# Optimization experiments

Measured on AMD Instinct MI355X. Metric: run time of the kernel, lower is better.

Reference implementation:

```python
import jax, jax.numpy as jnp
import numpy as np

VOCAB = 50001; W2V = 300; S2V = 256; HID = 256; COUT = 256; NTAG = 4; NHEADS = 5
N_POSTS = 2048; SEQ = 64


def mha(x, wqkv, bqkv, wo, bo, h):
    # torch nn.MultiheadAttention (batch_first, eval mode, no mask)
    n, s, d = x.shape
    hd = d // h
    qkv = x @ wqkv.T + bqkv                      # [n, s, 3d]
    q, k, v = jnp.split(qkv, 3, axis=-1)
    rs = lambda t: t.reshape(n, s, h, hd).transpose(0, 2, 1, 3)  # [n, h, s, hd]
    q, k, v = rs(q), rs(k), rs(v)
    att = jax.nn.softmax(jnp.einsum('nhqd,nhkd->nhqk', q, k) * (hd ** -0.5), axis=-1)
    o = jnp.einsum('nhqk,nhkd->nhqd', att, v).transpose(0, 2, 1, 3).reshape(n, s, d)
    return o @ wo.T + bo


def gcn_conv(x, ei, w, b):
    n = x.shape[0]
    loops = jnp.arange(n)
    src = jnp.concatenate([ei[0], loops])
    dst = jnp.concatenate([ei[1], loops])
    deg = jax.ops.segment_sum(jnp.ones(dst.shape[0], dtype=x.dtype), dst, num_segments=n)
    dinv = jnp.where(deg > 0, jax.lax.rsqrt(deg), 0.0)
    norm = dinv[src] * dinv[dst]                 # [E+n]
    h = x @ w.T                                  # [n, out]
    return jax.ops.segment_sum(norm[:, None] * h[src], dst, num_segments=n) + b


def gcn_branch(x, ei, root, w1, b1, w2, b2):
    # GCN.forward: conv1 -> cat root feat -> relu -> conv2 -> relu -> cat conv1 root -> mean
    n = x.shape[0]
    c1 = gcn_conv(x, ei, w1, b1)                 # [n, HID]
    post_root = jnp.broadcast_to(x[root], (n, x.shape[1]))
    c2_in = jax.nn.relu(jnp.concatenate([c1, post_root], axis=1))
    c2 = jax.nn.relu(gcn_conv(c2_in, ei, w2, b2))
    c1_root = jnp.broadcast_to(c1[root], (n, c1.shape[1]))
    feat = jnp.concatenate([c1_root, c2], axis=1)  # [n, HID+COUT]
    return jnp.mean(feat, axis=0).reshape(1, -1)


def setup_inputs() -> dict:
    key = jax.random.key(0)
    ks = jax.random.split(key, 16)
    p = lambda i, shp, sc=0.02: jax.random.normal(ks[i], shp, dtype=jnp.float32) * sc
    return {
        'nodeText': jax.random.randint(ks[0], (N_POSTS, SEQ), 0, VOCAB),
        'edgeIndexTD': jax.random.randint(ks[1], (2, N_POSTS - 1), 0, N_POSTS),
        'edgeIndexBU': jax.random.randint(ks[2], (2, N_POSTS - 1), 0, N_POSTS),
        'threadIndex': 0,
        'mission': 1,
        'embed_w': p(3, (VOCAB, W2V), 1.0),
        'in_proj_w': p(4, (3 * W2V, W2V)),
        'in_proj_b': jnp.zeros((3 * W2V,), jnp.float32),
        'out_proj_w': p(5, (W2V, W2V)),
        'out_proj_b': jnp.zeros((W2V,), jnp.float32),
        's2v_w': p(6, (S2V, W2V)),
        's2v_b': jnp.zeros((S2V,), jnp.float32),
        'td_w1': p(7, (HID, S2V)), 'td_b1': jnp.zeros((HID,), jnp.float32),
        'td_w2': p(8, (COUT, HID + S2V)), 'td_b2': jnp.zeros((COUT,), jnp.float32),
        'bu_w1': p(9, (HID, S2V)), 'bu_b1': jnp.zeros((HID,), jnp.float32),
        'bu_w2': p(10, (COUT, HID + S2V)), 'bu_b2': jnp.zeros((COUT,), jnp.float32),
        'fc_w': p(11, (NTAG, (COUT + HID) * 2)),
        'fc_b': jnp.zeros((NTAG,), jnp.float32),
    }


def reference(nodeText, edgeIndexTD, edgeIndexBU, threadIndex, mission,
              embed_w, in_proj_w, in_proj_b, out_proj_w, out_proj_b,
              s2v_w, s2v_b, td_w1, td_b1, td_w2, td_b2,
              bu_w1, bu_b1, bu_w2, bu_b2, fc_w, fc_b):
    # ABGCN.forward, mission == 1 (rumor/BiGCN path), eval mode (dropout off)
    nf = embed_w[nodeText]                                  # [N, S, W2V]
    nf = mha(nf, in_proj_w, in_proj_b, out_proj_w, out_proj_b, NHEADS)
    nf = jnp.tanh(nf @ s2v_w.T + s2v_b)                     # [N, S, S2V]
    s2v = nf[:, 0, :]                                       # first token per post
    td = gcn_branch(s2v, edgeIndexTD, threadIndex, td_w1, td_b1, td_w2, td_b2)
    bu = gcn_branch(s2v, edgeIndexBU, threadIndex, bu_w1, bu_b1, bu_w2, bu_b2)
    return jnp.concatenate([td, bu], axis=1) @ fc_w.T + fc_b  # [1, NTAG]
```

## Files before the change

kernel.cpp:

```cpp
#include <hip/hip_runtime.h>

#define NPOSTS 2048
#define SEQ 64
#define W2V 300
#define NH 5
#define HD 60
#define S2VD 256
#define HIDD 256
#define NEDGE 2047
#define UDIM 1500

#define GLOAD_LDS(g, l) \
    __builtin_amdgcn_global_load_lds((const __attribute__((address_space(1))) void*)(g), \
                                     (__attribute__((address_space(3))) void*)(l), 16, 0, 0)

__global__ __launch_bounds__(320) void k_wfoldA(
    const float* __restrict__ Ws, const float* __restrict__ Wo,
    const float* __restrict__ bo, const float* __restrict__ bs,
    float* __restrict__ WsWo, float* __restrict__ bias3A)
{
    const int r0 = blockIdx.x * 16;
    const int tid = threadIdx.x;
    __shared__ float sT[W2V][16];
    for (int i = tid; i < 16 * W2V; i += 320) {
        int r = i / W2V, k = i % W2V;
        sT[k][r] = Ws[(size_t)(r0 + r) * W2V + k];
    }
    __syncthreads();
    if (tid <= W2V) {
        float a[16];
        #pragma unroll
        for (int r = 0; r < 16; ++r) a[r] = 0.f;
        for (int k = 0; k < W2V; ++k) {
            float wv = (tid < W2V) ? Wo[(size_t)k * W2V + tid] : bo[k];
            const float4* s4 = reinterpret_cast<const float4*>(&sT[k][0]);
            float4 q0 = s4[0], q1 = s4[1], q2 = s4[2], q3 = s4[3];
            float qq[16] = {q0.x,q0.y,q0.z,q0.w, q1.x,q1.y,q1.z,q1.w,
                            q2.x,q2.y,q2.z,q2.w, q3.x,q3.y,q3.z,q3.w};
            #pragma unroll
            for (int r = 0; r < 16; ++r) a[r] = fmaf(wv, qq[r], a[r]);
        }
        if (tid < W2V) {
            #pragma unroll
            for (int r = 0; r < 16; ++r) WsWo[(size_t)(r0 + r) * W2V + tid] = a[r];
        } else {
            #pragma unroll
            for (int r = 0; r < 16; ++r) bias3A[r0 + r] = bs[r0 + r] + a[r];
        }
    }
}

__global__ __launch_bounds__(320) void k_wfold2(
    const float* __restrict__ WsWo, const float* __restrict__ Wqkv, const float* __restrict__ bqkv,
    float* __restrict__ Wfold, float* __restrict__ bpart)
{
    const int r0 = blockIdx.x * 16;
    const int h = blockIdx.y;
    const int tid = threadIdx.x;
    __shared__ float sT[HD][16];
    for (int i = tid; i < 16 * HD; i += 320) {
        int r = i / HD, d = i % HD;
        sT[d][r] = WsWo[(size_t)(r0 + r) * W2V + h * HD + d];
    }
    __syncthreads();
    if (tid <= W2V) {
        float a[16];
        #pragma unroll
        for (int r = 0; r < 16; ++r) a[r] = 0.f;
        for (int d = 0; d < HD; ++d) {
            float wv = (tid < W2V) ? Wqkv[(size_t)(2 * W2V + h * HD + d) * W2V + tid]
                                   : bqkv[2 * W2V + h * HD + d];
            const float4* s4 = reinterpret_cast<const float4*>(&sT[d][0]);
            float4 q0 = s4[0], q1 = s4[1], q2 = s4[2], q3 = s4[3];
            float qq[16] = {q0.x,q0.y,q0.z,q0.w, q1.x,q1.y,q1.z,q1.w,
                            q2.x,q2.y,q2.z,q2.w, q3.x,q3.y,q3.z,q3.w};
            #pragma unroll
            for (int r = 0; r < 16; ++r) a[r] = fmaf(wv, qq[r], a[r]);
        }
        if (tid < W2V) {
            #pragma unroll
            for (int r = 0; r < 16; ++r)
                Wfold[(size_t)(r0 + r) * UDIM + h * W2V + tid] = a[r];
        } else {
            #pragma unroll
            for (int r = 0; r < 16; ++r) bpart[h * S2VD + r0 + r] = a[r];
        }
    }
}

__global__ __launch_bounds__(320) void k_q(
    const int* __restrict__ nodeText, const float* __restrict__ embed_w,
    const float* __restrict__ Wqkv, const float* __restrict__ bqkv,
    float* __restrict__ Qout)
{
    const int r0 = blockIdx.x * 8;
    const int tid = threadIdx.x;
    __shared__ int stok[8];
    __shared__ float sE[8][W2V];
    if (tid < 8) stok[tid] = nodeText[(size_t)(r0 + tid) * SEQ];
    __syncthreads();
    for (int i = tid; i < 8 * 75; i += 320) {
        int r = i / 75, c4 = i % 75;
        *reinterpret_cast<float4*>(&sE[r][c4 * 4]) =
            *reinterpret_cast<const float4*>(embed_w + (size_t)stok[r] * W2V + c4 * 4);
    }
    __syncthreads();
    if (tid < W2V) {
        const float4* w4p = reinterpret_cast<const float4*>(Wqkv + (size_t)tid * W2V);
        float b = bqkv[tid];
        float a[8];
        #pragma unroll
        for (int r = 0; r < 8; ++r) a[r] = b;
        for (int c4 = 0; c4 < 75; ++c4) {
            float4 w4 = w4p[c4];
            #pragma unroll
            for (int r = 0; r < 8; ++r) {
                float4 v = *reinterpret_cast<const float4*>(&sE[r][c4 * 4]);
                a[r] = fmaf(w4.x, v.x, a[r]);
                a[r] = fmaf(w4.y, v.y, a[r]);
                a[r] = fmaf(w4.z, v.z, a[r]);
                a[r] = fmaf(w4.w, v.w, a[r]);
            }
        }
        #pragma unroll
        for (int r = 0; r < 8; ++r) Qout[(size_t)(r0 + r) * W2V + tid] = a[r];
    }
}

__global__ __launch_bounds__(320) void k_u(
    const float* __restrict__ Q, const float* __restrict__ Wqkv, float* __restrict__ uout)
{
    const int r0 = blockIdx.x * 16;
    const int h = blockIdx.y;
    const int tid = threadIdx.x;
    __shared__ float sT[HD][16];
    for (int i = tid; i < 16 * HD; i += 320) {
        int r = i / HD, d = i % HD;
        sT[d][r] = Q[(size_t)(r0 + r) * W2V + h * HD + d];
    }
    __syncthreads();
    if (tid < W2V) {
        float a[16];
        #pragma unroll
        for (int r = 0; r < 16; ++r) a[r] = 0.f;
        for (int d = 0; d < HD; ++d) {
            float wv = Wqkv[(size_t)(W2V + h * HD + d) * W2V + tid];
            const float4* s4 = reinterpret_cast<const float4*>(&sT[d][0]);
            float4 q0 = s4[0], q1 = s4[1], q2 = s4[2], q3 = s4[3];
            float qq[16] = {q0.x,q0.y,q0.z,q0.w, q1.x,q1.y,q1.z,q1.w,
                            q2.x,q2.y,q2.z,q2.w, q3.x,q3.y,q3.z,q3.w};
            #pragma unroll
            for (int r = 0; r < 16; ++r) a[r] = fmaf(wv, qq[r], a[r]);
        }
        #pragma unroll
        for (int r = 0; r < 16; ++r)
            uout[(size_t)(r0 + r) * UDIM + h * W2V + tid] = a[r];
    }
}

__global__ __launch_bounds__(512) void k_att(
    const int* __restrict__ nodeText, const float* __restrict__ embed_w,
    float* __restrict__ ue)
{
    __shared__ float sE[2 * SEQ * W2V];
    __shared__ float satt[2][NH][SEQ];
    __shared__ int   stoks[2][SEQ];

    const int p0 = blockIdx.x * 2;
    const int tid = threadIdx.x;
    const int wave = tid >> 6, lane = tid & 63;

    if (tid < 2 * SEQ) stoks[tid >> 6][tid & 63] = nodeText[(size_t)p0 * SEQ + tid];
    __syncthreads();

    #pragma unroll 3
    for (int it = 0; it < 18; ++it) {
        int i = it * 512 + tid;
        int pp = i / 4800, idx = i % 4800;
        int row = idx / 75, c4 = idx - row * 75;
        const float* src = embed_w + (size_t)stoks[pp][row] * W2V + c4 * 4;
        GLOAD_LDS(src, &sE[i * 4]);
    }
    if (wave < 6) {
        int i = 18 * 512 + tid;
        int pp = i / 4800, idx = i % 4800;
        int row = idx / 75, c4 = idx - row * 75;
        const float* src = embed_w + (size_t)stoks[pp][row] * W2V + c4 * 4;
        GLOAD_LDS(src, &sE[i * 4]);
    }
    asm volatile("s_waitcnt vmcnt(0)" ::: "memory");
    __syncthreads();

    const float SC = 0.12909944487358056f;
    for (int task = wave; task < 2 * NH; task += 8) {
        int pp = task / NH, h = task - pp * NH;
        const float4* u4 = reinterpret_cast<const float4*>(ue + (size_t)(p0 + pp) * UDIM + h * W2V);
        const float* er = &sE[(pp * SEQ + lane) * W2V];
        float acc = 0.f;
        #pragma unroll 5
        for (int c4 = 0; c4 < 75; ++c4) {
            float4 uv = u4[c4];
            float4 ev = *reinterpret_cast<const float4*>(er + c4 * 4);
            acc = fmaf(uv.x, ev.x, acc);
            acc = fmaf(uv.y, ev.y, acc);
            acc = fmaf(uv.z, ev.z, acc);
            acc = fmaf(uv.w, ev.w, acc);
        }
        float ex = expf(acc * SC);
        float l = ex;
        #pragma unroll
        for (int off = 32; off > 0; off >>= 1) l += __shfl_xor(l, off);
        satt[pp][h][lane] = ex / l;
    }
    __syncthreads();

    for (int t = tid; t < 2 * NH * 75; t += 512) {
        int pp = t / 375, r = t - pp * 375;
        int h = r / 75, c4 = r - h * 75;
        const float* att = &satt[pp][h][0];
        const float* eb = &sE[pp * SEQ * W2V + c4 * 4];
        float4 a = make_float4(0.f, 0.f, 0.f, 0.f);
        #pragma unroll 4
        for (int j = 0; j < SEQ; ++j) {
            float av = att[j];
            float4 ev = *reinterpret_cast<const float4*>(eb + j * W2V);
            a.x = fmaf(av, ev.x, a.x);
            a.y = fmaf(av, ev.y, a.y);
            a.z = fmaf(av, ev.z, a.z);
            a.w = fmaf(av, ev.w, a.w);
        }
        *reinterpret_cast<float4*>(ue + (size_t)(p0 + pp) * UDIM + h * W2V + c4 * 4) = a;
    }
}

__global__ __launch_bounds__(256) void k_s2v(
    const float* __restrict__ e, const float* __restrict__ Wfold,
    const float* __restrict__ bias3A, const float* __restrict__ bpart,
    float* __restrict__ s2v_out)
{
    const int r0 = blockIdx.x * 8;
    const int t = threadIdx.x;
    __shared__ float se[8][W2V];
    float a[8];
    #pragma unroll
    for (int r = 0; r < 8; ++r) a[r] = 0.f;
    const float bias = bias3A[t] + bpart[t] + bpart[256 + t] + bpart[512 + t]
                     + bpart[768 + t] + bpart[1024 + t];
    const float4* w4p = reinterpret_cast<const float4*>(Wfold + (size_t)t * UDIM);
    for (int ch = 0; ch < 5; ++ch) {
        __syncthreads();
        for (int i = t; i < 8 * 75; i += 256) {
            int r = i / 75, c4 = i % 75;
            *reinterpret_cast<float4*>(&se[r][c4 * 4]) =
                *reinterpret_cast<const float4*>(e + (size_t)(r0 + r) * UDIM + ch * W2V + c4 * 4);
        }
        __syncthreads();
        for (int c4 = 0; c4 < 75; ++c4) {
            float4 w4 = w4p[ch * 75 + c4];
            #pragma unroll
            for (int r = 0; r < 8; ++r) {
                float4 v = *reinterpret_cast<const float4*>(&se[r][c4 * 4]);
                a[r] = fmaf(w4.x, v.x, a[r]);
                a[r] = fmaf(w4.y, v.y, a[r]);
                a[r] = fmaf(w4.z, v.z, a[r]);
                a[r] = fmaf(w4.w, v.w, a[r]);
            }
        }
    }
    #pragma unroll
    for (int r = 0; r < 8; ++r)
        s2v_out[(size_t)(r0 + r) * S2VD + t] = tanhf(a[r] + bias);
}


__global__ __launch_bounds__(256) void k_deg(
    const int* __restrict__ eiTD, const int* __restrict__ eiBU, int* __restrict__ deg)
{
    const int b = blockIdx.y;
    const int* ei = b ? eiBU : eiTD;
    int e = blockIdx.x * 256 + threadIdx.x;
    if (e < NEDGE) atomicAdd(&deg[b * NPOSTS + ei[NEDGE + e]], 1);
}

__global__ __launch_bounds__(256) void k_gemm1(
    const float* __restrict__ x, const float* __restrict__ wtd, const float* __restrict__ wbu,
    const float* __restrict__ btd, const float* __restrict__ bbu, const int* __restrict__ deg,
    float* __restrict__ hout, float* __restrict__ cout_)
{
    const int b = blockIdx.y;
    const float* w = b ? wbu : wtd;
    const float* bias = b ? bbu : btd;
    float* hb = hout + (size_t)b * NPOSTS * HIDD;
    float* cb = cout_ + (size_t)b * NPOSTS * HIDD;
    const int* dg = deg + b * NPOSTS;
    const int r0 = blockIdx.x * 16;
    const int tid = threadIdx.x;
    __shared__ float sx[16][S2VD];
    for (int i = tid; i < 16 * S2VD; i += 256)
        sx[i / S2VD][i % S2VD] = x[(size_t)(r0 + i / S2VD) * S2VD + (i % S2VD)];
    __syncthreads();
    float acc[16];
    #pragma unroll
    for (int r = 0; r < 16; ++r) acc[r] = 0.f;
    const float4* wr4 = reinterpret_cast<const float4*>(w + (size_t)tid * S2VD);
    for (int c4 = 0; c4 < 64; ++c4) {
        float4 w4 = wr4[c4];
        #pragma unroll
        for (int r = 0; r < 16; ++r) {
            const float4 v = *reinterpret_cast<const float4*>(&sx[r][c4 * 4]);
            acc[r] = fmaf(w4.x, v.x, acc[r]);
            acc[r] = fmaf(w4.y, v.y, acc[r]);
            acc[r] = fmaf(w4.z, v.z, acc[r]);
            acc[r] = fmaf(w4.w, v.w, acc[r]);
        }
    }
    float bv = bias[tid];
    #pragma unroll
    for (int r = 0; r < 16; ++r) {
        int n = r0 + r;
        float dinv = 1.f / (float)(dg[n] + 1);
        hb[(size_t)n * HIDD + tid] = acc[r];
        cb[(size_t)n * HIDD + tid] = bv + acc[r] * dinv;
    }
}

__global__ __launch_bounds__(256) void k_gemm2(
    const float* __restrict__ c1, const float* __restrict__ w2td, const float* __restrict__ w2bu,
    const float* __restrict__ btd, const float* __restrict__ bbu, const int* __restrict__ deg,
    const float* __restrict__ rootv, float* __restrict__ hout, float* __restrict__ cout_)
{
    const int b = blockIdx.y;
    const float* w = b ? w2bu : w2td;
    const float* bias = b ? bbu : btd;
    const float* xin = c1 + (size_t)b * NPOSTS * HIDD;
    float* hb = hout + (size_t)b * NPOSTS * HIDD;
    float* cb = cout_ + (size_t)b * NPOSTS * HIDD;
    const int* dg = deg + b * NPOSTS;
    const int r0 = blockIdx.x * 16;
    const int tid = threadIdx.x;
    __shared__ float sx[16][HIDD];
    for (int i = tid; i < 16 * HIDD; i += 256)
        sx[i / HIDD][i % HIDD] = fmaxf(xin[(size_t)(r0 + i / HIDD) * HIDD + (i % HIDD)], 0.f);
    __syncthreads();
    float acc[16];
    const float rv = rootv[b * HIDD + tid];
    #pragma unroll
    for (int r = 0; r < 16; ++r) acc[r] = rv;
    const float4* wr4 = reinterpret_cast<const float4*>(w + (size_t)tid * 512);
    for (int c4 = 0; c4 < 64; ++c4) {
        float4 w4 = wr4[c4];
        #pragma unroll
        for (int r = 0; r < 16; ++r) {
            const float4 v = *reinterpret_cast<const float4*>(&sx[r][c4 * 4]);
            acc[r] = fmaf(w4.x, v.x, acc[r]);
            acc[r] = fmaf(w4.y, v.y, acc[r]);
            acc[r] = fmaf(w4.z, v.z, acc[r]);
            acc[r] = fmaf(w4.w, v.w, acc[r]);
        }
    }
    float bv = bias[tid];
    #pragma unroll
    for (int r = 0; r < 16; ++r) {
        int n = r0 + r;
        float dinv = 1.f / (float)(dg[n] + 1);
        hb[(size_t)n * HIDD + tid] = acc[r];
        cb[(size_t)n * HIDD + tid] = bv + acc[r] * dinv;
    }
}

__global__ __launch_bounds__(256) void k_scat(
    const int* __restrict__ eiTD, const int* __restrict__ eiBU,
    const float* __restrict__ h, const int* __restrict__ deg, float* __restrict__ cacc)
{
    const int b = blockIdx.y, e = blockIdx.x, tid = threadIdx.x;
    const int* ei = b ? eiBU : eiTD;
    const int s = ei[e], d = ei[NEDGE + e];
    const int* dg = deg + b * NPOSTS;
    float norm = rsqrtf((float)(dg[s] + 1)) * rsqrtf((float)(dg[d] + 1));
    const float* hb = h + (size_t)b * NPOSTS * HIDD;
    float* cb = cacc + (size_t)b * NPOSTS * HIDD;
    atomicAdd(&cb[(size_t)d * HIDD + tid], norm * hb[(size_t)s * HIDD + tid]);
}

__global__ __launch_bounds__(256) void k_root(
    const float* __restrict__ s2v, const float* __restrict__ c1,
    const float* __restrict__ w2td, const float* __restrict__ w2bu,
    const int* __restrict__ rootPtr, float* __restrict__ rootv, float* __restrict__ c1root)
{
    const int b = blockIdx.y, tid = threadIdx.x;
    const float* w2 = b ? w2bu : w2td;
    const int root = rootPtr[0];
    __shared__ float sx[S2VD];
    sx[tid] = fmaxf(s2v[(size_t)root * S2VD + tid], 0.f);
    __syncthreads();
    const float* cb = c1 + (size_t)b * NPOSTS * HIDD;
    c1root[b * HIDD + tid] = cb[(size_t)root * HIDD + tid];
    const float* wr = w2 + (size_t)tid * 512 + 256;
    float acc = 0.f;
    #pragma unroll 4
    for (int c = 0; c < S2VD; ++c) acc = fmaf(wr[c], sx[c], acc);
    rootv[b * HIDD + tid] = acc;
}

__global__ __launch_bounds__(256) void k_reduce(
    const float* __restrict__ cacc, float* __restrict__ msum)
{
    const int b = blockIdx.y, tid = threadIdx.x;
    const int base = blockIdx.x * 32;
    const float* cb = cacc + (size_t)b * NPOSTS * HIDD;
    float local = 0.f;
    #pragma unroll 4
    for (int r = 0; r < 32; ++r) local += fmaxf(cb[(size_t)(base + r) * HIDD + tid], 0.f);
    atomicAdd(&msum[b * HIDD + tid], local);
}

__global__ __launch_bounds__(256) void k_final(
    const float* __restrict__ c1root, const float* __restrict__ msum,
    const float* __restrict__ fc_w, const float* __restrict__ fc_b, float* __restrict__ outp)
{
    const int tid = threadIdx.x;
    __shared__ float sf[1024];
    for (int k = tid; k < 1024; k += 256) {
        int seg = k >> 8, idx = k & 255;
        float v;
        if (seg == 0)      v = c1root[idx];
        else if (seg == 1) v = msum[idx] * (1.f / (float)NPOSTS);
        else if (seg == 2) v = c1root[256 + idx];
        else               v = msum[256 + idx] * (1.f / (float)NPOSTS);
        sf[k] = v;
    }
    __syncthreads();
    const int t = tid >> 6, lane = tid & 63;
    float part = 0.f;
    for (int k = lane; k < 1024; k += 64) part = fmaf(fc_w[t * 1024 + k], sf[k], part);
    #pragma unroll
    for (int off = 32; off > 0; off >>= 1) part += __shfl_down(part, off);
    if (lane == 0) outp[t] = part + fc_b[t];
}

extern "C" void kernel_launch(void* const* d_in, const int* in_sizes, int n_in,
                              void* d_out, int out_size, void* d_ws, size_t ws_size,
                              hipStream_t stream) {
    (void)in_sizes; (void)n_in; (void)out_size; (void)ws_size;

    const int*   nodeText   = (const int*)d_in[0];
    const int*   eiTD       = (const int*)d_in[1];
    const int*   eiBU       = (const int*)d_in[2];
    const int*   threadIdxP = (const int*)d_in[3];
    const float* embed_w    = (const float*)d_in[5];
    const float* in_proj_w  = (const float*)d_in[6];
    const float* in_proj_b  = (const float*)d_in[7];
    const float* out_proj_w = (const float*)d_in[8];
    const float* out_proj_b = (const float*)d_in[9];
    const float* s2v_w      = (const float*)d_in[10];
    const float* s2v_b      = (const float*)d_in[11];
    const float* td_w1      = (const float*)d_in[12];
    const float* td_b1      = (const float*)d_in[13];
    const float* td_w2      = (const float*)d_in[14];
    const float* td_b2      = (const float*)d_in[15];
    const float* bu_w1      = (const float*)d_in[16];
    const float* bu_b1      = (const float*)d_in[17];
    const float* bu_w2      = (const float*)d_in[18];
    const float* bu_b2      = (const float*)d_in[19];
    const float* fc_w       = (const float*)d_in[20];
    const float* fc_b       = (const float*)d_in[21];
    float* outp = (float*)d_out;

    char* w = (char*)d_ws;
    int*   deg    = (int*)w;
    float* msum   = (float*)(w + 16384);
    float* rootv  = (float*)(w + 16384 + 2048);
    float* c1root = (float*)(w + 16384 + 4096);
    float* s2v    = (float*)(w + 24576);
    float* hbuf   = (float*)(w + 24576 + 2097152);
    float* cbuf   = (float*)(w + 24576 + 2097152 + 4194304);
    float* Qbuf   = (float*)(w + 24576 + 2097152 + 4194304 + 4194304);
    float* uebuf  = (float*)(w + 24576 + 2097152 + 4194304 + 4194304 + 2457600);

    float* Wfold  = hbuf;
    float* WsWo   = cbuf;
    float* bias3A = cbuf + 256 * 300;
    float* bpart  = bias3A + 256;

    hipMemsetAsync(d_ws, 0, 16384 + 2048, stream);

    k_deg<<<dim3((NEDGE + 255) / 256, 2), 256, 0, stream>>>(eiTD, eiBU, deg);
    k_wfoldA<<<16, 320, 0, stream>>>(s2v_w, out_proj_w, out_proj_b, s2v_b, WsWo, bias3A);
    k_wfold2<<<dim3(16, 5), 320, 0, stream>>>(WsWo, in_proj_w, in_proj_b, Wfold, bpart);

    k_q  <<<NPOSTS / 8, 320, 0, stream>>>(nodeText, embed_w, in_proj_w, in_proj_b, Qbuf);
    k_u  <<<dim3(NPOSTS / 16, 5), 320, 0, stream>>>(Qbuf, in_proj_w, uebuf);
    k_att<<<NPOSTS / 2, 512, 0, stream>>>(nodeText, embed_w, uebuf);
    k_s2v<<<NPOSTS / 8, 256, 0, stream>>>(uebuf, Wfold, bias3A, bpart, s2v);

    k_gemm1<<<dim3(NPOSTS / 16, 2), 256, 0, stream>>>(s2v, td_w1, bu_w1, td_b1, bu_b1, deg,
                                                      hbuf, cbuf);
    k_scat<<<dim3(NEDGE, 2), 256, 0, stream>>>(eiTD, eiBU, hbuf, deg, cbuf);

    k_root<<<dim3(1, 2), 256, 0, stream>>>(s2v, cbuf, td_w2, bu_w2, threadIdxP, rootv, c1root);

    k_gemm2<<<dim3(NPOSTS / 16, 2), 256, 0, stream>>>(cbuf, td_w2, bu_w2, td_b2, bu_b2, deg,
                                                      rootv, hbuf, cbuf);
    k_scat<<<dim3(NEDGE, 2), 256, 0, stream>>>(eiTD, eiBU, hbuf, deg, cbuf);

    k_reduce<<<dim3(NPOSTS / 32, 2), 256, 0, stream>>>(cbuf, msum);

    k_final<<<1, 256, 0, stream>>>(c1root, msum, fc_w, fc_b, outp);
}
```

Before: 354.9 us.

## Transpose weights and split K across thread groups in k_q and k_s2v GEMMs

The folded s2v weight is now stored transposed, and a transposed copy of the Q projection weight is added, so that each thread's weight loads are coalesced across the block. k_q and k_s2v stop staging activations in shared memory and read them straight from global memory as float4. The reduction dimension is split across three thread groups whose partial sums are combined through shared memory. This targets strided per-thread weight reads and low occupancy, at the cost of an extra transpose kernel, larger 900- and 768-thread blocks, and redundant global reads of activations.

```diff
diff --git a/kernel.cpp b/kernel.cpp
--- a/kernel.cpp
+++ b/kernel.cpp
@@ -52,7 +52,7 @@
 
 __global__ __launch_bounds__(320) void k_wfold2(
     const float* __restrict__ WsWo, const float* __restrict__ Wqkv, const float* __restrict__ bqkv,
-    float* __restrict__ Wfold, float* __restrict__ bpart)
+    float* __restrict__ WfoldT, float* __restrict__ bpart)
 {
     const int r0 = blockIdx.x * 16;
     const int h = blockIdx.y;
@@ -80,7 +80,7 @@
         if (tid < W2V) {
             #pragma unroll
             for (int r = 0; r < 16; ++r)
-                Wfold[(size_t)(r0 + r) * UDIM + h * W2V + tid] = a[r];
+                WfoldT[(size_t)(h * W2V + tid) * S2VD + (r0 + r)] = a[r];
         } else {
             #pragma unroll
             for (int r = 0; r < 16; ++r) bpart[h * S2VD + r0 + r] = a[r];
@@ -88,42 +88,95 @@
     }
 }
 
-__global__ __launch_bounds__(320) void k_q(
+__global__ __launch_bounds__(256) void k_wqT(
+    const float* __restrict__ W, float* __restrict__ WT)
+{
+    int i = blockIdx.x * 256 + threadIdx.x;
+    if (i < W2V * W2V) {
+        int r = i / W2V, c = i - r * W2V;
+        WT[(size_t)c * W2V + r] = W[i];
+    }
+}
+
+__global__ __launch_bounds__(900) void k_q(
     const int* __restrict__ nodeText, const float* __restrict__ embed_w,
-    const float* __restrict__ Wqkv, const float* __restrict__ bqkv,
+    const float* __restrict__ WqT, const float* __restrict__ bqkv,
     float* __restrict__ Qout)
 {
-    const int r0 = blockIdx.x * 8;
-    const int tid = threadIdx.x;
-    __shared__ int stok[8];
-    __shared__ float sE[8][W2V];
-    if (tid < 8) stok[tid] = nodeText[(size_t)(r0 + tid) * SEQ];
-    __syncthreads();
-    for (int i = tid; i < 8 * 75; i += 320) {
-        int r = i / 75, c4 = i % 75;
-        *reinterpret_cast<float4*>(&sE[r][c4 * 4]) =
-            *reinterpret_cast<const float4*>(embed_w + (size_t)stok[r] * W2V + c4 * 4);
-    }
-    __syncthreads();
-    if (tid < W2V) {
-        const float4* w4p = reinterpret_cast<const float4*>(Wqkv + (size_t)tid * W2V);
-        float b = bqkv[tid];
-        float a[8];
-        #pragma unroll
-        for (int r = 0; r < 8; ++r) a[r] = b;
-        for (int c4 = 0; c4 < 75; ++c4) {
-            float4 w4 = w4p[c4];
-            #pragma unroll
-            for (int r = 0; r < 8; ++r) {
-                float4 v = *reinterpret_cast<const float4*>(&sE[r][c4 * 4]);
-                a[r] = fmaf(w4.x, v.x, a[r]);
-                a[r] = fmaf(w4.y, v.y, a[r]);
-                a[r] = fmaf(w4.z, v.z, a[r]);
-                a[r] = fmaf(w4.w, v.w, a[r]);
-            }
-        }
-        #pragma unroll
-        for (int r = 0; r < 8; ++r) Qout[(size_t)(r0 + r) * W2V + tid] = a[r];
+    __shared__ float part[2][W2V * 9];
+    const int p0 = blockIdx.x * 8;
+    const int tid = threadIdx.x;
+    const int t = tid % W2V;
+    const int kg = tid / W2V;
+
+    const int tok0 = nodeText[(size_t)(p0 + 0) * SEQ];
+    const int tok1 = nodeText[(size_t)(p0 + 1) * SEQ];
+    const int tok2 = nodeText[(size_t)(p0 + 2) * SEQ];
+    const int tok3 = nodeText[(size_t)(p0 + 3) * SEQ];
+    const int tok4 = nodeText[(size_t)(p0 + 4) * SEQ];
+    const int tok5 = nodeText[(size_t)(p0 + 5) * SEQ];
+    const int tok6 = nodeText[(size_t)(p0 + 6) * SEQ];
+    const int tok7 = nodeText[(size_t)(p0 + 7) * SEQ];
+    const float* er0 = embed_w + (size_t)tok0 * W2V + kg * 100;
+    const float* er1 = embed_w + (size_t)tok1 * W2V + kg * 100;
+    const float* er2 = embed_w + (size_t)tok2 * W2V + kg * 100;
+    const float* er3 = embed_w + (size_t)tok3 * W2V + kg * 100;
+    const float* er4 = embed_w + (size_t)tok4 * W2V + kg * 100;
+    const float* er5 = embed_w + (size_t)tok5 * W2V + kg * 100;
+    const float* er6 = embed_w + (size_t)tok6 * W2V + kg * 100;
+    const float* er7 = embed_w + (size_t)tok7 * W2V + kg * 100;
+
+    float a0 = 0.f, a1 = 0.f, a2 = 0.f, a3 = 0.f, a4 = 0.f, a5 = 0.f, a6 = 0.f, a7 = 0.f;
+    const float* wp = WqT + (size_t)(kg * 100) * W2V + t;
+    for (int k4 = 0; k4 < 25; ++k4) {
+        const float w0 = wp[(size_t)(4 * k4 + 0) * W2V];
+        const float w1 = wp[(size_t)(4 * k4 + 1) * W2V];
+        const float w2 = wp[(size_t)(4 * k4 + 2) * W2V];
+        const float w3 = wp[(size_t)(4 * k4 + 3) * W2V];
+        const float4 e0 = *reinterpret_cast<const float4*>(er0 + 4 * k4);
+        const float4 e1 = *reinterpret_cast<const float4*>(er1 + 4 * k4);
+        const float4 e2 = *reinterpret_cast<const float4*>(er2 + 4 * k4);
+        const float4 e3 = *reinterpret_cast<const float4*>(er3 + 4 * k4);
+        const float4 e4 = *reinterpret_cast<const float4*>(er4 + 4 * k4);
+        const float4 e5 = *reinterpret_cast<const float4*>(er5 + 4 * k4);
+        const float4 e6 = *reinterpret_cast<const float4*>(er6 + 4 * k4);
+        const float4 e7 = *reinterpret_cast<const float4*>(er7 + 4 * k4);
+        a0 = fmaf(w0, e0.x, a0); a0 = fmaf(w1, e0.y, a0); a0 = fmaf(w2, e0.z, a0); a0 = fmaf(w3, e0.w, a0);
+        a1 = fmaf(w0, e1.x, a1); a1 = fmaf(w1, e1.y, a1); a1 = fmaf(w2, e1.z, a1); a1 = fmaf(w3, e1.w, a1);
+        a2 = fmaf(w0, e2.x, a2); a2 = fmaf(w1, e2.y, a2); a2 = fmaf(w2, e2.z, a2); a2 = fmaf(w3, e2.w, a2);
+        a3 = fmaf(w0, e3.x, a3); a3 = fmaf(w1, e3.y, a3); a3 = fmaf(w2, e3.z, a3); a3 = fmaf(w3, e3.w, a3);
+        a4 = fmaf(w0, e4.x, a4); a4 = fmaf(w1, e4.y, a4); a4 = fmaf(w2, e4.z, a4); a4 = fmaf(w3, e4.w, a4);
+        a5 = fmaf(w0, e5.x, a5); a5 = fmaf(w1, e5.y, a5); a5 = fmaf(w2, e5.z, a5); a5 = fmaf(w3, e5.w, a5);
+        a6 = fmaf(w0, e6.x, a6); a6 = fmaf(w1, e6.y, a6); a6 = fmaf(w2, e6.z, a6); a6 = fmaf(w3, e6.w, a6);
+        a7 = fmaf(w0, e7.x, a7); a7 = fmaf(w1, e7.y, a7); a7 = fmaf(w2, e7.z, a7); a7 = fmaf(w3, e7.w, a7);
+    }
+
+    if (kg != 0) {
+        float* pp = &part[kg - 1][t * 9];
+        pp[0] = a0; pp[1] = a1; pp[2] = a2; pp[3] = a3;
+        pp[4] = a4; pp[5] = a5; pp[6] = a6; pp[7] = a7;
+    }
+    __syncthreads();
+    if (kg == 0) {
+        const float* q0p = &part[0][t * 9];
+        const float* q1p = &part[1][t * 9];
+        const float b = bqkv[t];
+        float r0v = a0 + q0p[0] + q1p[0] + b;
+        float r1v = a1 + q0p[1] + q1p[1] + b;
+        float r2v = a2 + q0p[2] + q1p[2] + b;
+        float r3v = a3 + q0p[3] + q1p[3] + b;
+        float r4v = a4 + q0p[4] + q1p[4] + b;
+        float r5v = a5 + q0p[5] + q1p[5] + b;
+        float r6v = a6 + q0p[6] + q1p[6] + b;
+        float r7v = a7 + q0p[7] + q1p[7] + b;
+        Qout[(size_t)(p0 + 0) * W2V + t] = r0v;
+        Qout[(size_t)(p0 + 1) * W2V + t] = r1v;
+        Qout[(size_t)(p0 + 2) * W2V + t] = r2v;
+        Qout[(size_t)(p0 + 3) * W2V + t] = r3v;
+        Qout[(size_t)(p0 + 4) * W2V + t] = r4v;
+        Qout[(size_t)(p0 + 5) * W2V + t] = r5v;
+        Qout[(size_t)(p0 + 6) * W2V + t] = r6v;
+        Qout[(size_t)(p0 + 7) * W2V + t] = r7v;
     }
 }
 
@@ -233,43 +286,71 @@
     }
 }
 
-__global__ __launch_bounds__(256) void k_s2v(
-    const float* __restrict__ e, const float* __restrict__ Wfold,
+__global__ __launch_bounds__(768) void k_s2v(
+    const float* __restrict__ e, const float* __restrict__ WfoldT,
     const float* __restrict__ bias3A, const float* __restrict__ bpart,
     float* __restrict__ s2v_out)
 {
-    const int r0 = blockIdx.x * 8;
-    const int t = threadIdx.x;
-    __shared__ float se[8][W2V];
-    float a[8];
-    #pragma unroll
-    for (int r = 0; r < 8; ++r) a[r] = 0.f;
-    const float bias = bias3A[t] + bpart[t] + bpart[256 + t] + bpart[512 + t]
-                     + bpart[768 + t] + bpart[1024 + t];
-    const float4* w4p = reinterpret_cast<const float4*>(Wfold + (size_t)t * UDIM);
-    for (int ch = 0; ch < 5; ++ch) {
-        __syncthreads();
-        for (int i = t; i < 8 * 75; i += 256) {
-            int r = i / 75, c4 = i % 75;
-            *reinterpret_cast<float4*>(&se[r][c4 * 4]) =
-                *reinterpret_cast<const float4*>(e + (size_t)(r0 + r) * UDIM + ch * W2V + c4 * 4);
-        }
-        __syncthreads();
-        for (int c4 = 0; c4 < 75; ++c4) {
-            float4 w4 = w4p[ch * 75 + c4];
-            #pragma unroll
-            for (int r = 0; r < 8; ++r) {
-                float4 v = *reinterpret_cast<const float4*>(&se[r][c4 * 4]);
-                a[r] = fmaf(w4.x, v.x, a[r]);
-                a[r] = fmaf(w4.y, v.y, a[r]);
-                a[r] = fmaf(w4.z, v.z, a[r]);
-                a[r] = fmaf(w4.w, v.w, a[r]);
-            }
-        }
-    }
-    #pragma unroll
-    for (int r = 0; r < 8; ++r)
-        s2v_out[(size_t)(r0 + r) * S2VD + t] = tanhf(a[r] + bias);
+    __shared__ float part[2][S2VD * 9];
+    const int p0 = blockIdx.x * 8;
+    const int tid = threadIdx.x;
+    const int t = tid & 255;
+    const int kg = tid >> 8;
+
+    const float* er0 = e + (size_t)(p0 + 0) * UDIM + kg * 500;
+    const float* er1 = e + (size_t)(p0 + 1) * UDIM + kg * 500;
+    const float* er2 = e + (size_t)(p0 + 2) * UDIM + kg * 500;
+    const float* er3 = e + (size_t)(p0 + 3) * UDIM + kg * 500;
+    const float* er4 = e + (size_t)(p0 + 4) * UDIM + kg * 500;
+    const float* er5 = e + (size_t)(p0 + 5) * UDIM + kg * 500;
+    const float* er6 = e + (size_t)(p0 + 6) * UDIM + kg * 500;
+    const float* er7 = e + (size_t)(p0 + 7) * UDIM + kg * 500;
+
+    float a0 = 0.f, a1 = 0.f, a2 = 0.f, a3 = 0.f, a4 = 0.f, a5 = 0.f, a6 = 0.f, a7 = 0.f;
+    const float* wp = WfoldT + (size_t)(kg * 500) * S2VD + t;
+    for (int k4 = 0; k4 < 125; ++k4) {
+        const float w0 = wp[(size_t)(4 * k4 + 0) * S2VD];
+        const float w1 = wp[(size_t)(4 * k4 + 1) * S2VD];
+        const float w2 = wp[(size_t)(4 * k4 + 2) * S2VD];
+        const float w3 = wp[(size_t)(4 * k4 + 3) * S2VD];
+        const float4 e0 = *reinterpret_cast<const float4*>(er0 + 4 * k4);
+        const float4 e1 = *reinterpret_cast<const float4*>(er1 + 4 * k4);
+        const float4 e2 = *reinterpret_cast<const float4*>(er2 + 4 * k4);
+        const float4 e3 = *reinterpret_cast<const float4*>(er3 + 4 * k4);
+        const float4 e4 = *reinterpret_cast<const float4*>(er4 + 4 * k4);
+        const float4 e5 = *reinterpret_cast<const float4*>(er5 + 4 * k4);
+        const float4 e6 = *reinterpret_cast<const float4*>(er6 + 4 * k4);
+        const float4 e7 = *reinterpret_cast<const float4*>(er7 + 4 * k4);
+        a0 = fmaf(w0, e0.x, a0); a0 = fmaf(w1, e0.y, a0); a0 = fmaf(w2, e0.z, a0); a0 = fmaf(w3, e0.w, a0);
+        a1 = fmaf(w0, e1.x, a1); a1 = fmaf(w1, e1.y, a1); a1 = fmaf(w2, e1.z, a1); a1 = fmaf(w3, e1.w, a1);
+        a2 = fmaf(w0, e2.x, a2); a2 = fmaf(w1, e2.y, a2); a2 = fmaf(w2, e2.z, a2); a2 = fmaf(w3, e2.w, a2);
+        a3 = fmaf(w0, e3.x, a3); a3 = fmaf(w1, e3.y, a3); a3 = fmaf(w2, e3.z, a3); a3 = fmaf(w3, e3.w, a3);
+        a4 = fmaf(w0, e4.x, a4); a4 = fmaf(w1, e4.y, a4); a4 = fmaf(w2, e4.z, a4); a4 = fmaf(w3, e4.w, a4);
+        a5 = fmaf(w0, e5.x, a5); a5 = fmaf(w1, e5.y, a5); a5 = fmaf(w2, e5.z, a5); a5 = fmaf(w3, e5.w, a5);
+        a6 = fmaf(w0, e6.x, a6); a6 = fmaf(w1, e6.y, a6); a6 = fmaf(w2, e6.z, a6); a6 = fmaf(w3, e6.w, a6);
+        a7 = fmaf(w0, e7.x, a7); a7 = fmaf(w1, e7.y, a7); a7 = fmaf(w2, e7.z, a7); a7 = fmaf(w3, e7.w, a7);
+    }
+
+    if (kg != 0) {
+        float* pp = &part[kg - 1][t * 9];
+        pp[0] = a0; pp[1] = a1; pp[2] = a2; pp[3] = a3;
+        pp[4] = a4; pp[5] = a5; pp[6] = a6; pp[7] = a7;
+    }
+    __syncthreads();
+    if (kg == 0) {
+        const float* q0p = &part[0][t * 9];
+        const float* q1p = &part[1][t * 9];
+        const float bias = bias3A[t] + bpart[t] + bpart[256 + t] + bpart[512 + t]
+                         + bpart[768 + t] + bpart[1024 + t];
+        s2v_out[(size_t)(p0 + 0) * S2VD + t] = tanhf(a0 + q0p[0] + q1p[0] + bias);
+        s2v_out[(size_t)(p0 + 1) * S2VD + t] = tanhf(a1 + q0p[1] + q1p[1] + bias);
+        s2v_out[(size_t)(p0 + 2) * S2VD + t] = tanhf(a2 + q0p[2] + q1p[2] + bias);
+        s2v_out[(size_t)(p0 + 3) * S2VD + t] = tanhf(a3 + q0p[3] + q1p[3] + bias);
+        s2v_out[(size_t)(p0 + 4) * S2VD + t] = tanhf(a4 + q0p[4] + q1p[4] + bias);
+        s2v_out[(size_t)(p0 + 5) * S2VD + t] = tanhf(a5 + q0p[5] + q1p[5] + bias);
+        s2v_out[(size_t)(p0 + 6) * S2VD + t] = tanhf(a6 + q0p[6] + q1p[6] + bias);
+        s2v_out[(size_t)(p0 + 7) * S2VD + t] = tanhf(a7 + q0p[7] + q1p[7] + bias);
+    }
 }
 
 
@@ -477,21 +558,23 @@
     float* Qbuf   = (float*)(w + 24576 + 2097152 + 4194304 + 4194304);
     float* uebuf  = (float*)(w + 24576 + 2097152 + 4194304 + 4194304 + 2457600);
 
-    float* Wfold  = hbuf;
+    float* WfoldT = hbuf;
     float* WsWo   = cbuf;
-    float* bias3A = cbuf + 256 * 300;
-    float* bpart  = bias3A + 256;
+    float* bias3A = cbuf + 76800;
+    float* bpart  = cbuf + 77056;
+    float* WqT    = cbuf + 78336;
 
     hipMemsetAsync(d_ws, 0, 16384 + 2048, stream);
 
     k_deg<<<dim3((NEDGE + 255) / 256, 2), 256, 0, stream>>>(eiTD, eiBU, deg);
     k_wfoldA<<<16, 320, 0, stream>>>(s2v_w, out_proj_w, out_proj_b, s2v_b, WsWo, bias3A);
-    k_wfold2<<<dim3(16, 5), 320, 0, stream>>>(WsWo, in_proj_w, in_proj_b, Wfold, bpart);
-
-    k_q  <<<NPOSTS / 8, 320, 0, stream>>>(nodeText, embed_w, in_proj_w, in_proj_b, Qbuf);
+    k_wfold2<<<dim3(16, 5), 320, 0, stream>>>(WsWo, in_proj_w, in_proj_b, WfoldT, bpart);
+    k_wqT<<<(W2V * W2V + 255) / 256, 256, 0, stream>>>(in_proj_w, WqT);
+
+    k_q  <<<NPOSTS / 8, 900, 0, stream>>>(nodeText, embed_w, WqT, in_proj_b, Qbuf);
     k_u  <<<dim3(NPOSTS / 16, 5), 320, 0, stream>>>(Qbuf, in_proj_w, uebuf);
     k_att<<<NPOSTS / 2, 512, 0, stream>>>(nodeText, embed_w, uebuf);
-    k_s2v<<<NPOSTS / 8, 256, 0, stream>>>(uebuf, Wfold, bias3A, bpart, s2v);
+    k_s2v<<<NPOSTS / 8, 768, 0, stream>>>(uebuf, WfoldT, bias3A, bpart, s2v);
 
     k_gemm1<<<dim3(NPOSTS / 16, 2), 256, 0, stream>>>(s2v, td_w1, bu_w1, td_b1, bu_b1, deg,
                                                       hbuf, cbuf);
```

Result: slower. 382.8 us (+7.9%).
